# Performance work log

Hardware: AMD Instinct MI355X
Metric: run time of the kernel (lower is better)

## Reference

```python
import jax, jax.numpy as jnp
import numpy as np

BASE_MASK_RATIO = 0.3


def setup_inputs() -> dict:
    key = jax.random.key(0)
    k1, k2, k3 = jax.random.split(key, 3)
    B, E = 32768, 1024
    embeds = jax.random.normal(k1, (B, E), dtype=jnp.float32)
    dynamic_factors = jax.random.uniform(k2, (B,), dtype=jnp.float32)
    mask_token = jax.random.normal(k3, (1, E), dtype=jnp.float32)
    return {"embeds": embeds, "dynamic_factors": dynamic_factors, "mask_token": mask_token}


def reference(embeds, dynamic_factors, mask_token):
    # Per row i: mask_ratio = base * factor_i; num_masked = max(int(E*ratio), 1)
    # choose num_masked positions uniformly without replacement, replace with mask_token.
    B, E = embeds.shape
    # int() in torch truncates -> floor for non-negative ratios
    num_masked = jnp.maximum(
        jnp.floor(E * BASE_MASK_RATIO * dynamic_factors).astype(jnp.int32), 1
    )  # [B]
    # on-device RNG replacing the per-row numpy choice: rank of uniform scores
    scores = jax.random.uniform(jax.random.key(42), (B, E))
    rank = jnp.argsort(jnp.argsort(scores, axis=1), axis=1)  # [B, E] ranks 0..E-1
    masked = rank < num_masked[:, None]  # True where token is replaced
    mask = jnp.where(masked, 0.0, 1.0).astype(embeds.dtype)  # 1 = keep, 0 = masked
    masked_embeds = embeds * mask + mask_token * (1.0 - mask)
    return masked_embeds, mask
```

## Files before the change

### kernel.cpp

```cpp
#include <hip/hip_runtime.h>
#include <stdint.h>


#define B_ROWS 32768
#define E_COLS 1024

__device__ __forceinline__ uint32_t rotl(uint32_t x, uint32_t d) {
    return (x << d) | (x >> (32u - d));
}

__device__ __forceinline__ uint32_t threefry2x32_xor(uint32_t c0, uint32_t c1) {
    const uint32_t ks0 = 0u;
    const uint32_t ks1 = 42u;
    const uint32_t ks2 = 0x1BD11BDAu ^ ks0 ^ ks1;
    uint32_t x0 = c0 + ks0;
    uint32_t x1 = c1 + ks1;
#define TF_ROUND(d) { x0 += x1; x1 = rotl(x1, d); x1 ^= x0; }
    TF_ROUND(13) TF_ROUND(15) TF_ROUND(26) TF_ROUND(6)
    x0 += ks1; x1 += ks2 + 1u;
    TF_ROUND(17) TF_ROUND(29) TF_ROUND(16) TF_ROUND(24)
    x0 += ks2; x1 += ks0 + 2u;
    TF_ROUND(13) TF_ROUND(15) TF_ROUND(26) TF_ROUND(6)
    x0 += ks0; x1 += ks1 + 3u;
    TF_ROUND(17) TF_ROUND(29) TF_ROUND(16) TF_ROUND(24)
    x0 += ks1; x1 += ks2 + 4u;
    TF_ROUND(13) TF_ROUND(15) TF_ROUND(26) TF_ROUND(6)
    x0 += ks2; x1 += ks0 + 5u;
#undef TF_ROUND
    return x0 ^ x1;
}

__global__ __launch_bounds__(256) void DynamicNodeMask_kernel(
    const float* __restrict__ embeds,
    const float* __restrict__ factors,
    const float* __restrict__ mask_token,
    float* __restrict__ out)
{
    const int t = threadIdx.x;
    const int r = blockIdx.x;

    __shared__ uint32_t s_hist[256];
    __shared__ uint32_t s_scan[256];
    __shared__ uint32_t s_cand_key[1024];
    __shared__ uint16_t s_cand_idx[1024];
    __shared__ uint8_t  s_flags[1024];
    __shared__ uint32_t s_b0, s_excl, s_c;

    uint32_t key4[4];
#pragma unroll
    for (int e = 0; e < 4; ++e) {
        uint32_t j = (uint32_t)t * 4u + (uint32_t)e;
        uint32_t n = (uint32_t)r * 1024u + j;
        key4[e] = threefry2x32_xor(0u, n) >> 9;
    }

    const float f = factors[r];
    int k = (int)floorf(307.2f * f);
    if (k < 1) k = 1;

    s_hist[t] = 0u;
    if (t == 0) { s_b0 = 256u; s_c = 0u; }
    __syncthreads();
#pragma unroll
    for (int e = 0; e < 4; ++e)
        atomicAdd(&s_hist[key4[e] >> 15], 1u);
    __syncthreads();

    const uint32_t h = s_hist[t];
    s_scan[t] = h;
    __syncthreads();
    for (int off = 1; off < 256; off <<= 1) {
        uint32_t add = (t >= off) ? s_scan[t - off] : 0u;
        __syncthreads();
        s_scan[t] += add;
        __syncthreads();
    }
    const uint32_t incl = s_scan[t];
    if (incl >= (uint32_t)k) atomicMin(&s_b0, (uint32_t)t);
    __syncthreads();
    const uint32_t b0 = s_b0;
    if ((uint32_t)t == b0) s_excl = incl - h;
    __syncthreads();
    const uint32_t excl = s_excl;
    const uint32_t kprime = (uint32_t)k - excl;

    uint32_t w = 0u;
#pragma unroll
    for (int e = 0; e < 4; ++e) {
        uint32_t j = (uint32_t)t * 4u + (uint32_t)e;
        uint32_t u = key4[e];
        uint32_t bin = u >> 15;
        if (bin < b0) w |= (1u << (8 * e));
        if (bin == b0) {
            uint32_t pos = atomicAdd(&s_c, 1u);
            s_cand_key[pos] = u;
            s_cand_idx[pos] = (uint16_t)j;
        }
    }
    ((uint32_t*)&s_flags[0])[t] = w;
    __syncthreads();

    const uint32_t c = s_c;
    for (uint32_t p = (uint32_t)t; p < c; p += 256u) {
        uint32_t up = s_cand_key[p];
        uint32_t jp = s_cand_idx[p];
        uint32_t rank = 0u;
        for (uint32_t q = 0; q < c; ++q) {
            uint32_t uq = s_cand_key[q];
            uint32_t jq = s_cand_idx[q];
            rank += (uq < up || (uq == up && jq < jp)) ? 1u : 0u;
        }
        s_flags[jp] = (rank < kprime) ? 1u : 0u;
    }
    __syncthreads();

    const float4 mtv = ((const float4*)mask_token)[t];
    const size_t half = (size_t)B_ROWS * (size_t)E_COLS;
    const size_t row = (size_t)r;
    const float4 ev = ((const float4*)(embeds + row * E_COLS))[t];
    const uint32_t wf = ((const uint32_t*)&s_flags[0])[t];
    const bool f0 = (wf & 0x000000FFu) != 0u;
    const bool f1 = (wf & 0x0000FF00u) != 0u;
    const bool f2 = (wf & 0x00FF0000u) != 0u;
    const bool f3 = (wf & 0xFF000000u) != 0u;
    float4 me, mk;
    me.x = f0 ? mtv.x : ev.x;  mk.x = f0 ? 0.0f : 1.0f;
    me.y = f1 ? mtv.y : ev.y;  mk.y = f1 ? 0.0f : 1.0f;
    me.z = f2 ? mtv.z : ev.z;  mk.z = f2 ? 0.0f : 1.0f;
    me.w = f3 ? mtv.w : ev.w;  mk.w = f3 ? 0.0f : 1.0f;
    ((float4*)(out + row * E_COLS))[t] = me;
    ((float4*)(out + half + row * E_COLS))[t] = mk;
}

extern "C" void kernel_launch(void* const* d_in, const int* in_sizes, int n_in,
                              void* d_out, int out_size, void* d_ws, size_t ws_size,
                              hipStream_t stream) {
    const float* embeds     = (const float*)d_in[0];
    const float* factors    = (const float*)d_in[1];
    const float* mask_token = (const float*)d_in[2];
    float* out = (float*)d_out;
    (void)in_sizes; (void)n_in; (void)d_ws; (void)ws_size; (void)out_size;

    dim3 grid(B_ROWS);
    dim3 block(256);
    DynamicNodeMask_kernel<<<grid, block, 0, stream>>>(embeds, factors, mask_token, out);
}
```

Baseline: 386.8 us.

## Process one row per wavefront with shuffle-based scan and serial candidate ranking

Changes the mapping from one row per 256-thread block to one row per 64-lane wavefront, four rows per block. The block-wide shared-memory scan with many barriers is replaced by a wave-level shuffle scan and a ballot to locate the threshold bin. Each lane now generates 16 keys and builds a 16-bit mask in registers. The cost is that every lane walks the full candidate list serially, O(c^2) per lane. Candidates are also capped at MAXC=256, which could silently drop candidates if a bin overflows.

```diff
diff --git a/kernel.cpp b/kernel.cpp
--- a/kernel.cpp
+++ b/kernel.cpp
@@ -4,17 +4,18 @@
 
 #define B_ROWS 32768
 #define E_COLS 1024
+#define MAXC 256
 
 __device__ __forceinline__ uint32_t rotl(uint32_t x, uint32_t d) {
     return (x << d) | (x >> (32u - d));
 }
 
-__device__ __forceinline__ uint32_t threefry2x32_xor(uint32_t c0, uint32_t c1) {
+__device__ __forceinline__ uint32_t threefry_xor(uint32_t n) {
     const uint32_t ks0 = 0u;
     const uint32_t ks1 = 42u;
     const uint32_t ks2 = 0x1BD11BDAu ^ ks0 ^ ks1;
-    uint32_t x0 = c0 + ks0;
-    uint32_t x1 = c1 + ks1;
+    uint32_t x0 = 0u;
+    uint32_t x1 = n + ks1;
 #define TF_ROUND(d) { x0 += x1; x1 = rotl(x1, d); x1 ^= x0; }
     TF_ROUND(13) TF_ROUND(15) TF_ROUND(26) TF_ROUND(6)
     x0 += ks1; x1 += ks2 + 1u;
@@ -36,100 +37,117 @@
     const float* __restrict__ mask_token,
     float* __restrict__ out)
 {
-    const int t = threadIdx.x;
-    const int r = blockIdx.x;
+    const int t    = threadIdx.x;
+    const int w    = t >> 6;
+    const int lane = t & 63;
+    const int r    = blockIdx.x * 4 + w;
 
-    __shared__ uint32_t s_hist[256];
-    __shared__ uint32_t s_scan[256];
-    __shared__ uint32_t s_cand_key[1024];
-    __shared__ uint16_t s_cand_idx[1024];
-    __shared__ uint8_t  s_flags[1024];
-    __shared__ uint32_t s_b0, s_excl, s_c;
+    __shared__ uint32_t s_hist[4][256];
+    __shared__ uint32_t s_ckey[4][MAXC];
+    __shared__ uint16_t s_cidx[4][MAXC];
+    __shared__ uint32_t s_cnt[4];
 
-    uint32_t key4[4];
+    uint32_t u[16];
 #pragma unroll
-    for (int e = 0; e < 4; ++e) {
-        uint32_t j = (uint32_t)t * 4u + (uint32_t)e;
-        uint32_t n = (uint32_t)r * 1024u + j;
-        key4[e] = threefry2x32_xor(0u, n) >> 9;
+    for (int chunk = 0; chunk < 4; ++chunk)
+#pragma unroll
+        for (int e = 0; e < 4; ++e) {
+            uint32_t j = (uint32_t)chunk * 256u + (uint32_t)lane * 4u + (uint32_t)e;
+            u[chunk * 4 + e] = threefry_xor((uint32_t)r * 1024u + j) >> 9;
+        }
+
+#pragma unroll
+    for (int i = 0; i < 4; ++i) s_hist[w][lane + 64 * i] = 0u;
+    if (lane == 0) s_cnt[w] = 0u;
+    __syncthreads();
+
+#pragma unroll
+    for (int s = 0; s < 16; ++s)
+        atomicAdd(&s_hist[w][u[s] >> 15], 1u);
+    __syncthreads();
+
+    uint4 hv = *(const uint4*)&s_hist[w][lane * 4];
+    const uint32_t s0 = hv.x, s1 = hv.y, s2 = hv.z, s3 = hv.w;
+    const uint32_t L = s0 + s1 + s2 + s3;
+    uint32_t scan = L;
+#pragma unroll
+    for (int d = 1; d < 64; d <<= 1) {
+        uint32_t v = __shfl_up(scan, (unsigned)d, 64);
+        scan += (lane >= d) ? v : 0u;
     }
+    const uint32_t exclLane = scan - L;
 
     const float f = factors[r];
-    int k = (int)floorf(307.2f * f);
-    if (k < 1) k = 1;
+    int ki = (int)floorf(307.2f * f);
+    if (ki < 1) ki = 1;
+    const uint32_t k = (uint32_t)ki;
 
-    s_hist[t] = 0u;
-    if (t == 0) { s_b0 = 256u; s_c = 0u; }
-    __syncthreads();
+    const unsigned long long bal = __ballot(scan >= k);
+    const int l0 = __ffsll(bal) - 1;
+    const uint32_t i0 = exclLane + s0;
+    const uint32_t i1 = i0 + s1;
+    const uint32_t i2 = i1 + s2;
+    const uint32_t i3 = i2 + s3;
+    uint32_t b0loc, exloc;
+    if      (i0 >= k) { b0loc = (uint32_t)lane * 4u + 0u; exloc = i0 - s0; }
+    else if (i1 >= k) { b0loc = (uint32_t)lane * 4u + 1u; exloc = i1 - s1; }
+    else if (i2 >= k) { b0loc = (uint32_t)lane * 4u + 2u; exloc = i2 - s2; }
+    else              { b0loc = (uint32_t)lane * 4u + 3u; exloc = i3 - s3; }
+    const uint32_t b0     = (uint32_t)__shfl((int)b0loc, l0, 64);
+    const uint32_t excl   = (uint32_t)__shfl((int)exloc, l0, 64);
+    const uint32_t kprime = k - excl;
+
+    uint32_t m16 = 0u;
 #pragma unroll
-    for (int e = 0; e < 4; ++e)
-        atomicAdd(&s_hist[key4[e] >> 15], 1u);
-    __syncthreads();
-
-    const uint32_t h = s_hist[t];
-    s_scan[t] = h;
-    __syncthreads();
-    for (int off = 1; off < 256; off <<= 1) {
-        uint32_t add = (t >= off) ? s_scan[t - off] : 0u;
-        __syncthreads();
-        s_scan[t] += add;
-        __syncthreads();
-    }
-    const uint32_t incl = s_scan[t];
-    if (incl >= (uint32_t)k) atomicMin(&s_b0, (uint32_t)t);
-    __syncthreads();
-    const uint32_t b0 = s_b0;
-    if ((uint32_t)t == b0) s_excl = incl - h;
-    __syncthreads();
-    const uint32_t excl = s_excl;
-    const uint32_t kprime = (uint32_t)k - excl;
-
-    uint32_t w = 0u;
-#pragma unroll
-    for (int e = 0; e < 4; ++e) {
-        uint32_t j = (uint32_t)t * 4u + (uint32_t)e;
-        uint32_t u = key4[e];
-        uint32_t bin = u >> 15;
-        if (bin < b0) w |= (1u << (8 * e));
-        if (bin == b0) {
-            uint32_t pos = atomicAdd(&s_c, 1u);
-            s_cand_key[pos] = u;
-            s_cand_idx[pos] = (uint16_t)j;
+    for (int s = 0; s < 16; ++s) {
+        const uint32_t bin = u[s] >> 15;
+        if (bin < b0) m16 |= (1u << s);
+        else if (bin == b0) {
+            uint32_t pos = atomicAdd(&s_cnt[w], 1u);
+            if (pos < MAXC) {
+                uint32_t j = ((uint32_t)(s >> 2)) * 256u + (uint32_t)lane * 4u
+                           + (uint32_t)(s & 3);
+                s_ckey[w][pos] = u[s];
+                s_cidx[w][pos] = (uint16_t)j;
+            }
         }
-    }
-    ((uint32_t*)&s_flags[0])[t] = w;
-    __syncthreads();
-
-    const uint32_t c = s_c;
-    for (uint32_t p = (uint32_t)t; p < c; p += 256u) {
-        uint32_t up = s_cand_key[p];
-        uint32_t jp = s_cand_idx[p];
-        uint32_t rank = 0u;
-        for (uint32_t q = 0; q < c; ++q) {
-            uint32_t uq = s_cand_key[q];
-            uint32_t jq = s_cand_idx[q];
-            rank += (uq < up || (uq == up && jq < jp)) ? 1u : 0u;
-        }
-        s_flags[jp] = (rank < kprime) ? 1u : 0u;
     }
     __syncthreads();
 
-    const float4 mtv = ((const float4*)mask_token)[t];
+    uint32_t c = s_cnt[w];
+    if (c > MAXC) c = MAXC;
+    for (uint32_t p = 0; p < c; ++p) {
+        const uint32_t up = s_ckey[w][p];
+        const uint32_t jp = s_cidx[w][p];
+        uint32_t rank = 0u;
+        for (uint32_t q = 0; q < c; ++q) {
+            const uint32_t uq = s_ckey[w][q];
+            const uint32_t jq = s_cidx[w][q];
+            rank += (uq < up || (uq == up && jq < jp)) ? 1u : 0u;
+        }
+        if (rank < kprime && (((jp >> 2) & 63u) == (uint32_t)lane))
+            m16 |= 1u << ((jp >> 8) * 4u + (jp & 3u));
+    }
+
     const size_t half = (size_t)B_ROWS * (size_t)E_COLS;
-    const size_t row = (size_t)r;
-    const float4 ev = ((const float4*)(embeds + row * E_COLS))[t];
-    const uint32_t wf = ((const uint32_t*)&s_flags[0])[t];
-    const bool f0 = (wf & 0x000000FFu) != 0u;
-    const bool f1 = (wf & 0x0000FF00u) != 0u;
-    const bool f2 = (wf & 0x00FF0000u) != 0u;
-    const bool f3 = (wf & 0xFF000000u) != 0u;
-    float4 me, mk;
-    me.x = f0 ? mtv.x : ev.x;  mk.x = f0 ? 0.0f : 1.0f;
-    me.y = f1 ? mtv.y : ev.y;  mk.y = f1 ? 0.0f : 1.0f;
-    me.z = f2 ? mtv.z : ev.z;  mk.z = f2 ? 0.0f : 1.0f;
-    me.w = f3 ? mtv.w : ev.w;  mk.w = f3 ? 0.0f : 1.0f;
-    ((float4*)(out + row * E_COLS))[t] = me;
-    ((float4*)(out + half + row * E_COLS))[t] = mk;
+    const float4* mt4 = (const float4*)mask_token;
+#pragma unroll
+    for (int chunk = 0; chunk < 4; ++chunk) {
+        const size_t base = (size_t)r * E_COLS + (size_t)chunk * 256 + (size_t)lane * 4;
+        const float4 ev  = *(const float4*)(embeds + base);
+        const float4 mtv = mt4[chunk * 64 + lane];
+        const bool f0 = (m16 >> (chunk * 4 + 0)) & 1u;
+        const bool f1 = (m16 >> (chunk * 4 + 1)) & 1u;
+        const bool f2 = (m16 >> (chunk * 4 + 2)) & 1u;
+        const bool f3 = (m16 >> (chunk * 4 + 3)) & 1u;
+        float4 me, mk;
+        me.x = f0 ? mtv.x : ev.x;  mk.x = f0 ? 0.0f : 1.0f;
+        me.y = f1 ? mtv.y : ev.y;  mk.y = f1 ? 0.0f : 1.0f;
+        me.z = f2 ? mtv.z : ev.z;  mk.z = f2 ? 0.0f : 1.0f;
+        me.w = f3 ? mtv.w : ev.w;  mk.w = f3 ? 0.0f : 1.0f;
+        *(float4*)(out + base)        = me;
+        *(float4*)(out + half + base) = mk;
+    }
 }
 
 extern "C" void kernel_launch(void* const* d_in, const int* in_sizes, int n_in,
@@ -141,7 +159,7 @@
     float* out = (float*)d_out;
     (void)in_sizes; (void)n_in; (void)d_ws; (void)ws_size; (void)out_size;
 
-    dim3 grid(B_ROWS);
+    dim3 grid(B_ROWS / 4);
     dim3 block(256);
     DynamicNodeMask_kernel<<<grid, block, 0, stream>>>(embeds, factors, mask_token, out);
 }
```

Measured after the change: 372.6 us. 1.04x faster.
